# Kernel optimization log

Hardware: AMD Instinct MI355X
Metric: run time of the kernel (lower is better)

The kernel has to match this reference:

```python
import jax, jax.numpy as jnp
import numpy as np

N = 50000      # nodes
E = 800000     # edges
IN = 128       # in_channels
C = 32         # hidden_channels per head
H = 8          # heads
NC = 2         # num_classes
EPS = 1e-5     # batchnorm eps
SLOPE = 0.2    # leaky relu negative slope


def setup_inputs() -> dict:
    key = jax.random.key(0)
    ks = jax.random.split(key, 16)
    d = {}
    d["x"] = jax.random.normal(ks[0], (N, IN), dtype=jnp.float32)
    d["edge_index"] = jax.random.randint(ks[1], (2, E), 0, N, dtype=jnp.int64)
    # layer 0: IN -> H*C (concat)
    s0 = 1.0 / np.sqrt(IN)
    d["Wl0"] = jax.random.normal(ks[2], (IN, H * C), dtype=jnp.float32) * s0
    d["Wr0"] = jax.random.normal(ks[3], (IN, H * C), dtype=jnp.float32) * s0
    d["att0"] = jax.random.normal(ks[4], (H, C), dtype=jnp.float32) * (1.0 / np.sqrt(C))
    d["b0"] = jnp.zeros((H * C,), dtype=jnp.float32)
    d["g0"] = jnp.ones((H * C,), dtype=jnp.float32)
    d["be0"] = jnp.zeros((H * C,), dtype=jnp.float32)
    d["m0"] = jax.random.normal(ks[5], (H * C,), dtype=jnp.float32) * 0.1
    d["v0"] = jax.random.uniform(ks[6], (H * C,), dtype=jnp.float32, minval=0.5, maxval=1.5)
    # layer 1: H*C -> C (mean over heads, concat=False)
    s1 = 1.0 / np.sqrt(H * C)
    d["Wl1"] = jax.random.normal(ks[7], (H * C, H * C), dtype=jnp.float32) * s1
    d["Wr1"] = jax.random.normal(ks[8], (H * C, H * C), dtype=jnp.float32) * s1
    d["att1"] = jax.random.normal(ks[9], (H, C), dtype=jnp.float32) * (1.0 / np.sqrt(C))
    d["b1"] = jnp.zeros((C,), dtype=jnp.float32)
    d["g1"] = jnp.ones((C,), dtype=jnp.float32)
    d["be1"] = jnp.zeros((C,), dtype=jnp.float32)
    d["m1"] = jax.random.normal(ks[10], (C,), dtype=jnp.float32) * 0.1
    d["v1"] = jax.random.uniform(ks[11], (C,), dtype=jnp.float32, minval=0.5, maxval=1.5)
    # classifier C -> NC
    d["Wc"] = jax.random.normal(ks[12], (C, NC), dtype=jnp.float32) * (1.0 / np.sqrt(C))
    d["bc"] = jnp.zeros((NC,), dtype=jnp.float32)
    return d


def _gatv2_layer(x, src, dst, Wl, Wr, att, b, concat, num_nodes):
    # GATv2Conv (PyG semantics): x_l = source proj, x_r = target proj,
    # e_ij = att . LeakyReLU(x_l[j] + x_r[i]); softmax over incoming edges of i;
    # out_i = sum_j alpha_ij * x_l[j]. Self-loops are added (PyG default).
    nH, nC = att.shape
    xl = (x @ Wl).reshape(num_nodes, nH, nC)
    xr = (x @ Wr).reshape(num_nodes, nH, nC)
    e = xl[src] + xr[dst]                              # [E', H, C]
    e = jnp.where(e > 0, e, SLOPE * e)
    logits = jnp.einsum('ehc,hc->eh', e, att)          # [E', H]
    m = jax.ops.segment_max(logits, dst, num_segments=num_nodes)   # [N, H]
    ex = jnp.exp(logits - m[dst])
    denom = jax.ops.segment_sum(ex, dst, num_segments=num_nodes)   # [N, H]
    alpha = ex / denom[dst]                            # [E', H]
    msg = alpha[:, :, None] * xl[src]                  # [E', H, C]
    out = jax.ops.segment_sum(msg, dst, num_segments=num_nodes)    # [N, H, C]
    if concat:
        return out.reshape(num_nodes, nH * nC) + b
    return out.mean(axis=1) + b


def _bn(x, g, be, m, v):
    return (x - m) * jax.lax.rsqrt(v + EPS) * g + be


def reference(x, edge_index, Wl0, Wr0, att0, b0, g0, be0, m0, v0,
              Wl1, Wr1, att1, b1, g1, be1, m1, v1, Wc, bc):
    num_nodes = x.shape[0]
    loop = jnp.arange(num_nodes, dtype=edge_index.dtype)
    src = jnp.concatenate([edge_index[0], loop])
    dst = jnp.concatenate([edge_index[1], loop])
    h = _gatv2_layer(x, src, dst, Wl0, Wr0, att0, b0, True, num_nodes)
    h = _bn(h, g0, be0, m0, v0)
    h = jax.nn.elu(h)   # eval mode: dropout is identity
    h = _gatv2_layer(h, src, dst, Wl1, Wr1, att1, b1, False, num_nodes)
    h = _bn(h, g1, be1, m1, v1)
    return h @ Wc + bc
```

## Files before the change

### kernel.cpp

```cpp
#include <hip/hip_runtime.h>
#include <math.h>

#define N_NODES 50000
#define M_PAD   50048
#define E_EDGES 800000
#define IN_CH   128
#define C_CH    32
#define H_HEADS 8
#define HC      256
#define BN_EPS  1e-5f
#define SLOPE   0.2f

#define SCAN_CHUNK 512
#define SCAN_B     ((N_NODES + SCAN_CHUNK - 1) / SCAN_CHUNK)

typedef _Float16 f16x8 __attribute__((ext_vector_type(8)));
typedef _Float16 f16x4 __attribute__((ext_vector_type(4)));
typedef _Float16 f16x2 __attribute__((ext_vector_type(2)));
typedef float    f32x4 __attribute__((ext_vector_type(4)));


__global__ void k_init_deg(int* deg, int n) {
    int i = blockIdx.x * blockDim.x + threadIdx.x;
    if (i < n) deg[i] = 1;
}

__global__ void k_hist(const int* __restrict__ dst, int* deg, int e) {
    int i = blockIdx.x * blockDim.x + threadIdx.x;
    if (i < e) atomicAdd(&deg[dst[i]], 1);
}

__global__ __launch_bounds__(256) void k_scan_local(
        const int* __restrict__ deg, int* __restrict__ row_ptr,
        int* __restrict__ partials, int n) {
    __shared__ int sm[256];
    int t = threadIdx.x;
    int base = blockIdx.x * SCAN_CHUNK;
    int i0 = base + 2 * t, i1 = i0 + 1;
    int a = (i0 < n) ? deg[i0] : 0;
    int b = (i1 < n) ? deg[i1] : 0;
    int s = a + b;
    sm[t] = s;
    __syncthreads();
    #pragma unroll
    for (int off = 1; off < 256; off <<= 1) {
        int u = (t >= off) ? sm[t - off] : 0;
        __syncthreads();
        sm[t] += u;
        __syncthreads();
    }
    int excl = sm[t] - s;
    if (i0 < n) row_ptr[i0] = excl;
    if (i1 < n) row_ptr[i1] = excl + a;
    if (t == 255) partials[blockIdx.x] = sm[255];
}

__global__ __launch_bounds__(128) void k_scan_part(
        int* __restrict__ partials, int* __restrict__ row_ptr_n) {
    __shared__ int sm[128];
    int t = threadIdx.x;
    int v = (t < SCAN_B) ? partials[t] : 0;
    sm[t] = v;
    __syncthreads();
    #pragma unroll
    for (int off = 1; off < 128; off <<= 1) {
        int u = (t >= off) ? sm[t - off] : 0;
        __syncthreads();
        sm[t] += u;
        __syncthreads();
    }
    if (t < SCAN_B) partials[t] = sm[t] - v;
    if (t == 127) *row_ptr_n = sm[127];
}

__global__ void k_scan_add(int* __restrict__ row_ptr, int* __restrict__ cursor,
                           const int* __restrict__ partials, int n) {
    int i = blockIdx.x * blockDim.x + threadIdx.x;
    if (i < n) {
        int v = row_ptr[i] + partials[i / SCAN_CHUNK];
        row_ptr[i] = v;
        cursor[i] = v;
    }
}

__global__ void k_fill(const int* __restrict__ src, const int* __restrict__ dst,
                       int* cursor, int* csr_src, int e, int n) {
    int i = blockIdx.x * blockDim.x + threadIdx.x;
    if (i < e) {
        int d = dst[i];
        int p = atomicAdd(&cursor[d], 1);
        csr_src[p] = src[i];
    } else if (i < e + n) {
        int v = i - e;
        int p = atomicAdd(&cursor[v], 1);
        csr_src[p] = v;
    }
}


__global__ void k_split_w4(const float* __restrict__ Wl0, const float* __restrict__ Wr0,
                           const float* __restrict__ Wl1, const float* __restrict__ Wr1,
                           _Float16* __restrict__ W0lt, _Float16* __restrict__ W0rt,
                           _Float16* __restrict__ W1lt, _Float16* __restrict__ W1rt) {
    int t = blockIdx.x * blockDim.x + threadIdx.x;
    const float* W; _Float16* O; int K, rel;
    if (t < 32768)       { W = Wl0; O = W0lt; K = 128; rel = t; }
    else if (t < 65536)  { W = Wr0; O = W0rt; K = 128; rel = t - 32768; }
    else if (t < 131072) { W = Wl1; O = W1lt; K = 256; rel = t - 65536; }
    else if (t < 196608) { W = Wr1; O = W1rt; K = 256; rel = t - 131072; }
    else return;
    int n = rel / K, k = rel - n * K;
    O[rel] = (_Float16)W[(size_t)k * 256 + n];
}


#define BK  32
#define LDA 40

__device__ __forceinline__ f16x8 cvt_h8(float4 a, float4 b) {
    f16x8 v = { (_Float16)a.x, (_Float16)a.y, (_Float16)a.z, (_Float16)a.w,
                (_Float16)b.x, (_Float16)b.y, (_Float16)b.z, (_Float16)b.w };
    return v;
}

__global__ __launch_bounds__(256) void k_gemm_mfma(
        const _Float16* __restrict__ A16, const float* __restrict__ A32,
        const _Float16* __restrict__ W0t, const _Float16* __restrict__ W1t,
        _Float16* __restrict__ C0, _Float16* __restrict__ C1, int K) {
    const _Float16* Wt = blockIdx.z ? W1t : W0t;
    _Float16* C = blockIdx.z ? C1 : C0;
    __shared__ _Float16 As[128 * LDA];
    __shared__ _Float16 Bs[128 * LDA];
    int t = threadIdx.x;
    int lane = t & 63, wv = t >> 6;
    int quad = lane >> 4, r16 = lane & 15;
    size_t mBase = (size_t)blockIdx.x * 128;
    size_t nBase = (size_t)blockIdx.y * 128;
    int sr = t >> 2;
    int sc = (t & 3) * 8;
    f32x4 acc[2][8] = {};
    for (int k0 = 0; k0 < K; k0 += BK) {
        if (A32) {
            size_t r0 = mBase + sr, r1 = r0 + 64;
            float4 a0 = {0.f,0.f,0.f,0.f}, a1 = a0, b0 = a0, b1 = a0;
            if (r0 < N_NODES) {
                const float* g = A32 + r0 * K + k0 + sc;
                a0 = ((const float4*)g)[0];
                a1 = ((const float4*)g)[1];
            }
            if (r1 < N_NODES) {
                const float* g = A32 + r1 * K + k0 + sc;
                b0 = ((const float4*)g)[0];
                b1 = ((const float4*)g)[1];
            }
            *(f16x8*)&As[sr * LDA + sc]        = cvt_h8(a0, a1);
            *(f16x8*)&As[(sr + 64) * LDA + sc] = cvt_h8(b0, b1);
        } else {
            const _Float16* gA = A16 + (mBase + sr) * K + k0 + sc;
            *(f16x8*)&As[sr * LDA + sc]        = *(const f16x8*)gA;
            *(f16x8*)&As[(sr + 64) * LDA + sc] = *(const f16x8*)(gA + (size_t)64 * K);
        }
        const _Float16* gB = Wt + (nBase + sr) * K + k0 + sc;
        *(f16x8*)&Bs[sr * LDA + sc]        = *(const f16x8*)gB;
        *(f16x8*)&Bs[(sr + 64) * LDA + sc] = *(const f16x8*)(gB + (size_t)64 * K);
        __syncthreads();
        f16x8 av[2];
        #pragma unroll
        for (int mi = 0; mi < 2; ++mi) {
            int m = wv * 32 + mi * 16 + r16;
            av[mi] = *(f16x8*)&As[m * LDA + quad * 8];
        }
        #pragma unroll
        for (int ni = 0; ni < 8; ++ni) {
            int n = ni * 16 + r16;
            f16x8 bv = *(f16x8*)&Bs[n * LDA + quad * 8];
            #pragma unroll
            for (int mi = 0; mi < 2; ++mi)
                acc[mi][ni] = __builtin_amdgcn_mfma_f32_16x16x32_f16(av[mi], bv, acc[mi][ni], 0, 0, 0);
        }
        __syncthreads();
    }
    #pragma unroll
    for (int mi = 0; mi < 2; ++mi)
        #pragma unroll
        for (int r = 0; r < 4; ++r) {
            size_t row = mBase + wv * 32 + mi * 16 + quad * 4 + r;
            _Float16* cp = C + row * 256 + nBase + r16;
            #pragma unroll
            for (int ni = 0; ni < 8; ++ni)
                cp[ni * 16] = (_Float16)acc[mi][ni][r];
        }
}


__device__ __forceinline__ float edge_w16(f16x4 h, f16x4 xr, f16x4 att) {
    f16x4 e = h + xr;
    f16x4 es = e * (_Float16)SLOPE;
    f16x4 l = __builtin_elementwise_max(e, es);
#if __has_builtin(__builtin_amdgcn_fdot2)
    f16x2 l01 = __builtin_shufflevector(l, l, 0, 1);
    f16x2 l23 = __builtin_shufflevector(l, l, 2, 3);
    f16x2 a01 = __builtin_shufflevector(att, att, 0, 1);
    f16x2 a23 = __builtin_shufflevector(att, att, 2, 3);
    float p = __builtin_amdgcn_fdot2(l01, a01, 0.f, false);
    p = __builtin_amdgcn_fdot2(l23, a23, p, false);
#else
    float p = (float)l[0] * (float)att[0];
    p = fmaf((float)l[1], (float)att[1], p);
    p = fmaf((float)l[2], (float)att[2], p);
    p = fmaf((float)l[3], (float)att[3], p);
#endif
    p += __shfl_xor(p, 1);
    p += __shfl_xor(p, 2);
    p += __shfl_xor(p, 4);
    return __expf(p);
}

__device__ __forceinline__ float4 edge_accum(
        const f16x4* __restrict__ xl4, f16x4 xr_h, f16x4 att_h,
        const int* __restrict__ csr_src, int beg, int end, int lane) {
    const f16x4* xlp = xl4 + lane;
    float4 acc = {0.f, 0.f, 0.f, 0.f};
    float S = 0.f;
    int j = beg;
    for (; j + 4 <= end; j += 4) {
        int s0 = csr_src[j];
        int s1 = csr_src[j + 1];
        int s2 = csr_src[j + 2];
        int s3 = csr_src[j + 3];
        f16x4 h0 = xlp[(size_t)s0 * 64];
        f16x4 h1 = xlp[(size_t)s1 * 64];
        f16x4 h2 = xlp[(size_t)s2 * 64];
        f16x4 h3 = xlp[(size_t)s3 * 64];
        float w0 = edge_w16(h0, xr_h, att_h);
        float w1 = edge_w16(h1, xr_h, att_h);
        float w2 = edge_w16(h2, xr_h, att_h);
        float w3 = edge_w16(h3, xr_h, att_h);
        S += (w0 + w1) + (w2 + w3);
        acc.x = fmaf((float)h0[0], w0, acc.x); acc.y = fmaf((float)h0[1], w0, acc.y);
        acc.z = fmaf((float)h0[2], w0, acc.z); acc.w = fmaf((float)h0[3], w0, acc.w);
        acc.x = fmaf((float)h1[0], w1, acc.x); acc.y = fmaf((float)h1[1], w1, acc.y);
        acc.z = fmaf((float)h1[2], w1, acc.z); acc.w = fmaf((float)h1[3], w1, acc.w);
        acc.x = fmaf((float)h2[0], w2, acc.x); acc.y = fmaf((float)h2[1], w2, acc.y);
        acc.z = fmaf((float)h2[2], w2, acc.z); acc.w = fmaf((float)h2[3], w2, acc.w);
        acc.x = fmaf((float)h3[0], w3, acc.x); acc.y = fmaf((float)h3[1], w3, acc.y);
        acc.z = fmaf((float)h3[2], w3, acc.z); acc.w = fmaf((float)h3[3], w3, acc.w);
    }
    for (; j < end; ++j) {
        int s = csr_src[j];
        f16x4 hv = xlp[(size_t)s * 64];
        float w = edge_w16(hv, xr_h, att_h);
        S += w;
        acc.x = fmaf((float)hv[0], w, acc.x); acc.y = fmaf((float)hv[1], w, acc.y);
        acc.z = fmaf((float)hv[2], w, acc.z); acc.w = fmaf((float)hv[3], w, acc.w);
    }
    float inv = 1.f / S;
    acc.x *= inv; acc.y *= inv; acc.z *= inv; acc.w *= inv;
    return acc;
}

__device__ __forceinline__ f16x4 cvt_h4(float4 v) {
    f16x4 r = { (_Float16)v.x, (_Float16)v.y, (_Float16)v.z, (_Float16)v.w };
    return r;
}

__global__ __launch_bounds__(256) void k_edge0(
        const _Float16* __restrict__ xl, const _Float16* __restrict__ xr,
        const float* __restrict__ att,
        const int* __restrict__ row_ptr, const int* __restrict__ csr_src,
        const float* __restrict__ b0, const float* __restrict__ g0,
        const float* __restrict__ be0, const float* __restrict__ m0,
        const float* __restrict__ v0,
        _Float16* __restrict__ h0) {
    int lane = threadIdx.x & 63;
    int i = blockIdx.x * 4 + (threadIdx.x >> 6);
    const f16x4* xl4 = (const f16x4*)xl;
    f16x4 xr_h = ((const f16x4*)xr)[(size_t)i * 64 + lane];
    f16x4 att_h = cvt_h4(((const float4*)att)[lane]);
    int beg = row_ptr[i], end = row_ptr[i + 1];
    float4 r = edge_accum(xl4, xr_h, att_h, csr_src, beg, end, lane);
    float4 bb = ((const float4*)b0)[lane];
    float4 gg = ((const float4*)g0)[lane];
    float4 ee = ((const float4*)be0)[lane];
    float4 mm = ((const float4*)m0)[lane];
    float4 vv = ((const float4*)v0)[lane];
    float4 o;
    o.x = (r.x + bb.x - mm.x) * rsqrtf(vv.x + BN_EPS) * gg.x + ee.x;
    o.y = (r.y + bb.y - mm.y) * rsqrtf(vv.y + BN_EPS) * gg.y + ee.y;
    o.z = (r.z + bb.z - mm.z) * rsqrtf(vv.z + BN_EPS) * gg.z + ee.z;
    o.w = (r.w + bb.w - mm.w) * rsqrtf(vv.w + BN_EPS) * gg.w + ee.w;
    o.x = o.x > 0.f ? o.x : expm1f(o.x);
    o.y = o.y > 0.f ? o.y : expm1f(o.y);
    o.z = o.z > 0.f ? o.z : expm1f(o.z);
    o.w = o.w > 0.f ? o.w : expm1f(o.w);
    f16x4 hh = { (_Float16)o.x, (_Float16)o.y, (_Float16)o.z, (_Float16)o.w };
    ((f16x4*)h0)[(size_t)i * 64 + lane] = hh;
}

__global__ __launch_bounds__(256) void k_edge1(
        const _Float16* __restrict__ xl, const _Float16* __restrict__ xr,
        const float* __restrict__ att,
        const int* __restrict__ row_ptr, const int* __restrict__ csr_src,
        const float* __restrict__ b1, const float* __restrict__ g1,
        const float* __restrict__ be1, const float* __restrict__ m1,
        const float* __restrict__ v1,
        const float* __restrict__ Wc, const float* __restrict__ bc,
        float* __restrict__ out) {
    int lane = threadIdx.x & 63;
    int q = lane & 7;
    int i = blockIdx.x * 4 + (threadIdx.x >> 6);
    const f16x4* xl4 = (const f16x4*)xl;
    f16x4 xr_h = ((const f16x4*)xr)[(size_t)i * 64 + lane];
    f16x4 att_h = cvt_h4(((const float4*)att)[lane]);
    int beg = row_ptr[i], end = row_ptr[i + 1];
    float4 r = edge_accum(xl4, xr_h, att_h, csr_src, beg, end, lane);
    #pragma unroll
    for (int mask = 8; mask <= 32; mask <<= 1) {
        r.x += __shfl_xor(r.x, mask);
        r.y += __shfl_xor(r.y, mask);
        r.z += __shfl_xor(r.z, mask);
        r.w += __shfl_xor(r.w, mask);
    }
    float4 bb = ((const float4*)b1)[q];
    float4 gg = ((const float4*)g1)[q];
    float4 ee = ((const float4*)be1)[q];
    float4 mm = ((const float4*)m1)[q];
    float4 vv = ((const float4*)v1)[q];
    r.x = (r.x * 0.125f + bb.x - mm.x) * rsqrtf(vv.x + BN_EPS) * gg.x + ee.x;
    r.y = (r.y * 0.125f + bb.y - mm.y) * rsqrtf(vv.y + BN_EPS) * gg.y + ee.y;
    r.z = (r.z * 0.125f + bb.z - mm.z) * rsqrtf(vv.z + BN_EPS) * gg.z + ee.z;
    r.w = (r.w * 0.125f + bb.w - mm.w) * rsqrtf(vv.w + BN_EPS) * gg.w + ee.w;
    float4 wc0 = ((const float4*)Wc)[q * 2];
    float4 wc1 = ((const float4*)Wc)[q * 2 + 1];
    float o0 = r.x * wc0.x + r.y * wc0.z + r.z * wc1.x + r.w * wc1.z;
    float o1 = r.x * wc0.y + r.y * wc0.w + r.z * wc1.y + r.w * wc1.w;
    #pragma unroll
    for (int mask = 1; mask <= 4; mask <<= 1) {
        o0 += __shfl_xor(o0, mask);
        o1 += __shfl_xor(o1, mask);
    }
    if (lane == 0) {
        float2 ov = {o0 + bc[0], o1 + bc[1]};
        *(float2*)(out + (size_t)i * 2) = ov;
    }
}


extern "C" void kernel_launch(void* const* d_in, const int* in_sizes, int n_in,
                              void* d_out, int out_size, void* d_ws, size_t ws_size,
                              hipStream_t stream) {
    const float* x    = (const float*)d_in[0];
    const int*   ei   = (const int*)d_in[1];
    const float* Wl0  = (const float*)d_in[2];
    const float* Wr0  = (const float*)d_in[3];
    const float* att0 = (const float*)d_in[4];
    const float* b0   = (const float*)d_in[5];
    const float* g0   = (const float*)d_in[6];
    const float* be0  = (const float*)d_in[7];
    const float* m0   = (const float*)d_in[8];
    const float* v0   = (const float*)d_in[9];
    const float* Wl1  = (const float*)d_in[10];
    const float* Wr1  = (const float*)d_in[11];
    const float* att1 = (const float*)d_in[12];
    const float* b1   = (const float*)d_in[13];
    const float* g1   = (const float*)d_in[14];
    const float* be1  = (const float*)d_in[15];
    const float* m1   = (const float*)d_in[16];
    const float* v1   = (const float*)d_in[17];
    const float* Wc   = (const float*)d_in[18];
    const float* bc   = (const float*)d_in[19];
    float* out = (float*)d_out;

    const int N = N_NODES, E = E_EDGES;
    const int* srcp = ei;
    const int* dstp = ei + E;

    char* p = (char*)d_ws;
    _Float16* xlf = (_Float16*)p; p += (size_t)M_PAD * HC * 2;
    _Float16* xrf = (_Float16*)p; p += (size_t)M_PAD * HC * 2;
    _Float16* h0  = (_Float16*)p; p += (size_t)M_PAD * HC * 2;
    _Float16* W0lt = (_Float16*)p; p += (size_t)HC * IN_CH * 2;
    _Float16* W0rt = (_Float16*)p; p += (size_t)HC * IN_CH * 2;
    _Float16* W1lt = (_Float16*)p; p += (size_t)HC * HC * 2;
    _Float16* W1rt = (_Float16*)p; p += (size_t)HC * HC * 2;
    int* deg      = (int*)p;
    int* row_ptr  = deg + N;
    int* cursor   = row_ptr + (N + 1);
    int* partials = cursor + N;
    int* csr_src  = partials + ((SCAN_B + 3) & ~3);

    k_init_deg<<<(N + 255) / 256, 256, 0, stream>>>(deg, N);
    k_hist<<<(E + 255) / 256, 256, 0, stream>>>(dstp, deg, E);
    k_scan_local<<<SCAN_B, 256, 0, stream>>>(deg, row_ptr, partials, N);
    k_scan_part<<<1, 128, 0, stream>>>(partials, row_ptr + N);
    k_scan_add<<<(N + 255) / 256, 256, 0, stream>>>(row_ptr, cursor, partials, N);
    k_fill<<<(E + N + 255) / 256, 256, 0, stream>>>(srcp, dstp, cursor, csr_src, E, N);

    k_split_w4<<<768, 256, 0, stream>>>(Wl0, Wr0, Wl1, Wr1, W0lt, W0rt, W1lt, W1rt);

    dim3 ggrid(M_PAD / 128, 2, 2);
    k_gemm_mfma<<<ggrid, 256, 0, stream>>>(nullptr, x, W0lt, W0rt, xlf, xrf, IN_CH);
    k_edge0<<<N / 4, 256, 0, stream>>>(xlf, xrf, att0, row_ptr, csr_src,
                                       b0, g0, be0, m0, v0, h0);
    k_gemm_mfma<<<ggrid, 256, 0, stream>>>(h0, nullptr, W1lt, W1rt, xlf, xrf, HC);
    k_edge1<<<N / 4, 256, 0, stream>>>(xlf, xrf, att1, row_ptr, csr_src,
                                       b1, g1, be1, m1, v1, Wc, bc, out);
}
```

Measured before the change: 408.4 us.

## Fuse CSR build and weight conversion into one cooperative kernel with grid syncs

Replaces seven small launches (degree init, histogram, three scan stages, fill, weight transpose) with a single cooperative kernel of 1024 blocks that separates the phases with grid-wide syncs. The goal is to remove per-launch overhead and the gaps between the tiny preprocessing kernels. In exchange the work runs on a fixed grid with grid.sync barriers, and the scan is regrouped into 256-element chunks handled by a single block for the partials. It requires all 1024 blocks to be co-resident for the cooperative launch to succeed.

```diff
diff --git a/kernel.cpp b/kernel.cpp
--- a/kernel.cpp
+++ b/kernel.cpp
@@ -1,5 +1,8 @@
 #include <hip/hip_runtime.h>
+#include <hip/hip_cooperative_groups.h>
 #include <math.h>
+
+namespace cg = cooperative_groups;
 
 #define N_NODES 50000
 #define M_PAD   50048
@@ -11,8 +14,9 @@
 #define BN_EPS  1e-5f
 #define SLOPE   0.2f
 
-#define SCAN_CHUNK 512
-#define SCAN_B     ((N_NODES + SCAN_CHUNK - 1) / SCAN_CHUNK)
+#define CSR_BLOCKS  1024
+#define CSR_THREADS 256
+#define N_CHUNKS    ((N_NODES + CSR_THREADS - 1) / CSR_THREADS)
 
 typedef _Float16 f16x8 __attribute__((ext_vector_type(8)));
 typedef _Float16 f16x4 __attribute__((ext_vector_type(4)));
@@ -20,97 +24,82 @@
 typedef float    f32x4 __attribute__((ext_vector_type(4)));
 
 
-__global__ void k_init_deg(int* deg, int n) {
-    int i = blockIdx.x * blockDim.x + threadIdx.x;
-    if (i < n) deg[i] = 1;
-}
-
-__global__ void k_hist(const int* __restrict__ dst, int* deg, int e) {
-    int i = blockIdx.x * blockDim.x + threadIdx.x;
-    if (i < e) atomicAdd(&deg[dst[i]], 1);
-}
-
-__global__ __launch_bounds__(256) void k_scan_local(
-        const int* __restrict__ deg, int* __restrict__ row_ptr,
-        int* __restrict__ partials, int n) {
-    __shared__ int sm[256];
+__global__ void k_csr_prep(const int* __restrict__ src, const int* __restrict__ dst,
+                           const float* __restrict__ Wl0, const float* __restrict__ Wr0,
+                           const float* __restrict__ Wl1, const float* __restrict__ Wr1,
+                           _Float16* __restrict__ W0lt, _Float16* __restrict__ W0rt,
+                           _Float16* __restrict__ W1lt, _Float16* __restrict__ W1rt,
+                           int* __restrict__ deg, int* __restrict__ row_ptr,
+                           int* __restrict__ cursor, int* __restrict__ partials,
+                           int* __restrict__ csr_src) {
+    cg::grid_group grid = cg::this_grid();
+    __shared__ int sm[CSR_THREADS];
     int t = threadIdx.x;
-    int base = blockIdx.x * SCAN_CHUNK;
-    int i0 = base + 2 * t, i1 = i0 + 1;
-    int a = (i0 < n) ? deg[i0] : 0;
-    int b = (i1 < n) ? deg[i1] : 0;
-    int s = a + b;
-    sm[t] = s;
-    __syncthreads();
-    #pragma unroll
-    for (int off = 1; off < 256; off <<= 1) {
-        int u = (t >= off) ? sm[t - off] : 0;
+    int gid = blockIdx.x * CSR_THREADS + t;
+    const int gsz = CSR_BLOCKS * CSR_THREADS;
+
+    for (int i = gid; i < N_NODES; i += gsz) deg[i] = 1;
+    for (int w = gid; w < 196608; w += gsz) {
+        const float* W; _Float16* O; int K, rel;
+        if (w < 32768)       { W = Wl0; O = W0lt; K = 128; rel = w; }
+        else if (w < 65536)  { W = Wr0; O = W0rt; K = 128; rel = w - 32768; }
+        else if (w < 131072) { W = Wl1; O = W1lt; K = 256; rel = w - 65536; }
+        else                 { W = Wr1; O = W1rt; K = 256; rel = w - 131072; }
+        int n = rel / K, k = rel - n * K;
+        O[rel] = (_Float16)W[(size_t)k * 256 + n];
+    }
+    grid.sync();
+
+    for (int e = gid; e < E_EDGES; e += gsz) atomicAdd(&deg[dst[e]], 1);
+    grid.sync();
+
+    if (blockIdx.x < N_CHUNKS) {
+        int i = blockIdx.x * CSR_THREADS + t;
+        int v = (i < N_NODES) ? deg[i] : 0;
+        sm[t] = v;
         __syncthreads();
-        sm[t] += u;
+        #pragma unroll
+        for (int off = 1; off < CSR_THREADS; off <<= 1) {
+            int u = (t >= off) ? sm[t - off] : 0;
+            __syncthreads();
+            sm[t] += u;
+            __syncthreads();
+        }
+        if (i < N_NODES) row_ptr[i] = sm[t] - v;
+        if (t == CSR_THREADS - 1) partials[blockIdx.x] = sm[t];
+    }
+    grid.sync();
+
+    if (blockIdx.x == 0) {
+        int v = (t < N_CHUNKS) ? partials[t] : 0;
+        sm[t] = v;
         __syncthreads();
-    }
-    int excl = sm[t] - s;
-    if (i0 < n) row_ptr[i0] = excl;
-    if (i1 < n) row_ptr[i1] = excl + a;
-    if (t == 255) partials[blockIdx.x] = sm[255];
-}
-
-__global__ __launch_bounds__(128) void k_scan_part(
-        int* __restrict__ partials, int* __restrict__ row_ptr_n) {
-    __shared__ int sm[128];
-    int t = threadIdx.x;
-    int v = (t < SCAN_B) ? partials[t] : 0;
-    sm[t] = v;
-    __syncthreads();
-    #pragma unroll
-    for (int off = 1; off < 128; off <<= 1) {
-        int u = (t >= off) ? sm[t - off] : 0;
-        __syncthreads();
-        sm[t] += u;
-        __syncthreads();
-    }
-    if (t < SCAN_B) partials[t] = sm[t] - v;
-    if (t == 127) *row_ptr_n = sm[127];
-}
-
-__global__ void k_scan_add(int* __restrict__ row_ptr, int* __restrict__ cursor,
-                           const int* __restrict__ partials, int n) {
-    int i = blockIdx.x * blockDim.x + threadIdx.x;
-    if (i < n) {
-        int v = row_ptr[i] + partials[i / SCAN_CHUNK];
+        #pragma unroll
+        for (int off = 1; off < CSR_THREADS; off <<= 1) {
+            int u = (t >= off) ? sm[t - off] : 0;
+            __syncthreads();
+            sm[t] += u;
+            __syncthreads();
+        }
+        if (t < N_CHUNKS) partials[t] = sm[t] - v;
+        if (t == 0) row_ptr[N_NODES] = E_EDGES + N_NODES;
+    }
+    grid.sync();
+
+    for (int i = gid; i < N_NODES; i += gsz) {
+        int v = row_ptr[i] + partials[i >> 8];
         row_ptr[i] = v;
         cursor[i] = v;
     }
-}
-
-__global__ void k_fill(const int* __restrict__ src, const int* __restrict__ dst,
-                       int* cursor, int* csr_src, int e, int n) {
-    int i = blockIdx.x * blockDim.x + threadIdx.x;
-    if (i < e) {
-        int d = dst[i];
+    grid.sync();
+
+    for (int e = gid; e < E_EDGES + N_NODES; e += gsz) {
+        int s, d;
+        if (e < E_EDGES) { s = src[e]; d = dst[e]; }
+        else             { s = e - E_EDGES; d = s; }
         int p = atomicAdd(&cursor[d], 1);
-        csr_src[p] = src[i];
-    } else if (i < e + n) {
-        int v = i - e;
-        int p = atomicAdd(&cursor[v], 1);
-        csr_src[p] = v;
-    }
-}
-
-
-__global__ void k_split_w4(const float* __restrict__ Wl0, const float* __restrict__ Wr0,
-                           const float* __restrict__ Wl1, const float* __restrict__ Wr1,
-                           _Float16* __restrict__ W0lt, _Float16* __restrict__ W0rt,
-                           _Float16* __restrict__ W1lt, _Float16* __restrict__ W1rt) {
-    int t = blockIdx.x * blockDim.x + threadIdx.x;
-    const float* W; _Float16* O; int K, rel;
-    if (t < 32768)       { W = Wl0; O = W0lt; K = 128; rel = t; }
-    else if (t < 65536)  { W = Wr0; O = W0rt; K = 128; rel = t - 32768; }
-    else if (t < 131072) { W = Wl1; O = W1lt; K = 256; rel = t - 65536; }
-    else if (t < 196608) { W = Wr1; O = W1rt; K = 256; rel = t - 131072; }
-    else return;
-    int n = rel / K, k = rel - n * K;
-    O[rel] = (_Float16)W[(size_t)k * 256 + n];
+        csr_src[p] = s;
+    }
 }
 
 
@@ -371,9 +360,8 @@
     const float* bc   = (const float*)d_in[19];
     float* out = (float*)d_out;
 
-    const int N = N_NODES, E = E_EDGES;
     const int* srcp = ei;
-    const int* dstp = ei + E;
+    const int* dstp = ei + E_EDGES;
 
     char* p = (char*)d_ws;
     _Float16* xlf = (_Float16*)p; p += (size_t)M_PAD * HC * 2;
@@ -384,25 +372,29 @@
     _Float16* W1lt = (_Float16*)p; p += (size_t)HC * HC * 2;
     _Float16* W1rt = (_Float16*)p; p += (size_t)HC * HC * 2;
     int* deg      = (int*)p;
-    int* row_ptr  = deg + N;
-    int* cursor   = row_ptr + (N + 1);
-    int* partials = cursor + N;
-    int* csr_src  = partials + ((SCAN_B + 3) & ~3);
-
-    k_init_deg<<<(N + 255) / 256, 256, 0, stream>>>(deg, N);
-    k_hist<<<(E + 255) / 256, 256, 0, stream>>>(dstp, deg, E);
-    k_scan_local<<<SCAN_B, 256, 0, stream>>>(deg, row_ptr, partials, N);
-    k_scan_part<<<1, 128, 0, stream>>>(partials, row_ptr + N);
-    k_scan_add<<<(N + 255) / 256, 256, 0, stream>>>(row_ptr, cursor, partials, N);
-    k_fill<<<(E + N + 255) / 256, 256, 0, stream>>>(srcp, dstp, cursor, csr_src, E, N);
-
-    k_split_w4<<<768, 256, 0, stream>>>(Wl0, Wr0, Wl1, Wr1, W0lt, W0rt, W1lt, W1rt);
+    int* row_ptr  = deg + N_NODES;
+    int* cursor   = row_ptr + (N_NODES + 1);
+    int* partials = cursor + N_NODES;
+    int* csr_src  = partials + ((N_CHUNKS + 3) & ~3);
+
+    {
+        void* args[] = {
+            (void*)&srcp, (void*)&dstp,
+            (void*)&Wl0, (void*)&Wr0, (void*)&Wl1, (void*)&Wr1,
+            (void*)&W0lt, (void*)&W0rt, (void*)&W1lt, (void*)&W1rt,
+            (void*)&deg, (void*)&row_ptr, (void*)&cursor, (void*)&partials,
+            (void*)&csr_src,
+        };
+        hipLaunchCooperativeKernel((const void*)k_csr_prep,
+                                   dim3(CSR_BLOCKS), dim3(CSR_THREADS),
+                                   args, 0, stream);
+    }
 
     dim3 ggrid(M_PAD / 128, 2, 2);
     k_gemm_mfma<<<ggrid, 256, 0, stream>>>(nullptr, x, W0lt, W0rt, xlf, xrf, IN_CH);
-    k_edge0<<<N / 4, 256, 0, stream>>>(xlf, xrf, att0, row_ptr, csr_src,
-                                       b0, g0, be0, m0, v0, h0);
+    k_edge0<<<N_NODES / 4, 256, 0, stream>>>(xlf, xrf, att0, row_ptr, csr_src,
+                                             b0, g0, be0, m0, v0, h0);
     k_gemm_mfma<<<ggrid, 256, 0, stream>>>(h0, nullptr, W1lt, W1rt, xlf, xrf, HC);
-    k_edge1<<<N / 4, 256, 0, stream>>>(xlf, xrf, att1, row_ptr, csr_src,
-                                       b1, g1, be1, m1, v1, Wc, bc, out);
-}
+    k_edge1<<<N_NODES / 4, 256, 0, stream>>>(xlf, xrf, att1, row_ptr, csr_src,
+                                             b1, g1, be1, m1, v1, Wc, bc, out);
+}
```

Result: slower. 951.5 us (+133.0%).
